# Optimization experiments

Hardware: AMD Instinct MI355X
Metric: run time of the kernel (lower is better)

Reference implementation:

```python
import jax, jax.numpy as jnp
import numpy as np

N_ATOMS = 20
N_IN, N_EMB_N, N_EMB_E, N_H_N, N_H_E = 4, 128, 128, 256, 256


def lstm_seq(x, Wi, bi, Wh, bh):
    """x: [B, M, T, D] -> h sequence [B, M, T, H]. Gates stacked as (i,f,g,o).
    Equivalent to the per-gate nn.Linear pairs: bi/bh are the two bias vectors."""
    B, M, T, D = x.shape
    H = Wh.shape[0]
    # precompute all input-to-hidden projections in one big GEMM: [T,B,M,4H]
    xg = jnp.einsum('bmtd,dg->tbmg', x, Wi) + bi

    def step(carry, xg_t):
        c, h = carry
        g = xg_t + h @ Wh + bh  # [B,M,4H]
        i, f, gg, o = jnp.split(g, 4, axis=-1)
        i = jax.nn.sigmoid(i)
        f = jax.nn.sigmoid(f)
        gg = jnp.tanh(gg)
        o = jax.nn.sigmoid(o)
        c = f * c + i * gg
        h = o * jnp.tanh(c)
        return (c, h), h

    z = jnp.zeros((B, M, H), x.dtype)
    _, hs = jax.lax.scan(step, (z, z), xg)  # hs: [T,B,M,H]
    return jnp.transpose(hs, (1, 2, 0, 3))


def setup_inputs() -> dict:
    key = jax.random.key(0)
    ks = jax.random.split(key, 16)
    s = 0.05
    # fully-connected directed edges without self loops -> one-hot incidence
    send, rec = np.where(~np.eye(N_ATOMS, dtype=bool))
    eye = np.eye(N_ATOMS, dtype=np.float32)
    inp = {
        'X': jax.random.normal(ks[0], (16, N_ATOMS, 64, N_IN), jnp.float32),
        'rel_rec': jnp.asarray(eye[rec]),
        'rel_send': jnp.asarray(eye[send]),
        # motion embedding fc
        'Wm': jax.random.normal(ks[1], (N_IN, N_EMB_N), jnp.float32) * s,
        'bm': jnp.zeros((N_EMB_N,), jnp.float32),
        # motion LSTM (gates i,f,g,o stacked)
        'Wmi': jax.random.normal(ks[2], (N_EMB_N, 4 * N_H_N), jnp.float32) * s,
        'bmi': jnp.zeros((4 * N_H_N,), jnp.float32),
        'Wmh': jax.random.normal(ks[3], (N_H_N, 4 * N_H_N), jnp.float32) * s,
        'bmh': jnp.zeros((4 * N_H_N,), jnp.float32),
        # interaction embedding fc (in = 2*n_h_node)
        'We': jax.random.normal(ks[4], (2 * N_H_N, N_EMB_E), jnp.float32) * s,
        'be': jnp.zeros((N_EMB_E,), jnp.float32),
        # edge LSTM
        'Wei': jax.random.normal(ks[5], (N_EMB_E, 4 * N_H_E), jnp.float32) * s,
        'bei': jnp.zeros((4 * N_H_E,), jnp.float32),
        'Weh': jax.random.normal(ks[6], (N_H_E, 4 * N_H_E), jnp.float32) * s,
        'beh': jnp.zeros((4 * N_H_E,), jnp.float32),
        # output fc
        'Wf': jax.random.normal(ks[7], (N_H_E, 1), jnp.float32) * s,
        'bf': jnp.zeros((1,), jnp.float32),
    }
    return inp


def reference(X, rel_rec, rel_send, Wm, bm, Wmi, bmi, Wmh, bmh,
              We, be, Wei, bei, Weh, beh, Wf, bf):
    # Motion embedding on temporal deltas: [B,N,T-1,n_emb_node]
    dX = X[:, :, 1:, :] - X[:, :, :-1, :]
    em = dX @ Wm + bm
    # Motion LSTM, full sequence: [B,N,T-1,Hn]
    hm = lstm_seq(em, Wmi, bmi, Wmh, bmh)
    # Interaction embedding: gather per-edge sender/receiver node states
    senders = jnp.einsum('en,bnth->beth', rel_send, hm)
    receivers = jnp.einsum('en,bnth->beth', rel_rec, hm)
    edges = jnp.concatenate([senders, receivers], axis=-1)  # [B,E,T-1,2Hn]
    ea = edges @ We + be  # [B,E,T-1,n_emb_edge]
    # Edge LSTM, last hidden state: [B,E,He]
    he = lstm_seq(ea, Wei, bei, Weh, beh)[:, :, -1, :]
    # Edge scores -> dense adjacency via incidence matrices
    A = jax.nn.sigmoid(he @ Wf + bf)[..., 0]  # [B,E]
    Ad = jnp.einsum('en,be,em->bnm', rel_send, A, rel_rec)  # send^T diag(A) rec
    return 0.5 * (Ad + jnp.transpose(Ad, (0, 2, 1)))  # symmetrize
```

## Files before the change

### kernel.cpp

```cpp
#include <hip/hip_runtime.h>
#include <stdint.h>

#define NBATCH 16
#define NNODE  20
#define TSTEPS 63
#define NEDGE  380
#define HID    256
#define G4     1024
#define RS     280

typedef __bf16 bf16x8 __attribute__((ext_vector_type(8)));
typedef float  f32x4  __attribute__((ext_vector_type(4)));

__device__ __forceinline__ float bf2f(unsigned short u){
  union { unsigned int i; float f; } v; v.i = ((unsigned int)u) << 16; return v.f;
}
__device__ __forceinline__ unsigned short f2bf(float f){
  union { float f; unsigned int i; } v; v.f = f;
  return (unsigned short)((v.i + 0x7FFFu + ((v.i >> 16) & 1u)) >> 16);
}
__device__ __forceinline__ bf16x8 as_frag(uint4 v){
  union { uint4 u; bf16x8 b; } c; c.u = v; return c.b;
}
__device__ __forceinline__ float sigmf(float x){ return 1.0f/(1.0f+__expf(-x)); }
__device__ __forceinline__ float tanh_f(float x){ float e=__expf(2.0f*x); return (e-1.0f)/(e+1.0f); }

__device__ __forceinline__ unsigned long long load_ax(const unsigned long long* p){
  return __hip_atomic_load(p, __ATOMIC_RELAXED, __HIP_MEMORY_SCOPE_AGENT);
}
__device__ __forceinline__ void store_ax(unsigned long long* p, unsigned long long v){
  __hip_atomic_store(p, v, __ATOMIC_RELAXED, __HIP_MEMORY_SCOPE_AGENT);
}
__device__ __forceinline__ void wait_vm0(){ asm volatile("s_waitcnt vmcnt(0)" ::: "memory"); }

__global__ __launch_bounds__(256) void prep_a(
    const float* __restrict__ We, const float* __restrict__ Wei,
    const float* __restrict__ Wm, const float* __restrict__ Wmi,
    const float* __restrict__ bm, const float* __restrict__ bmi, const float* __restrict__ bmh,
    const float* __restrict__ be, const float* __restrict__ bei, const float* __restrict__ beh,
    float* __restrict__ Wse, float* __restrict__ Wre, float* __restrict__ WcmGI,
    float* __restrict__ bcmGI, float* __restrict__ bceGI,
    float* __restrict__ Afin, unsigned int* __restrict__ ectr, unsigned int* __restrict__ mctr){
  int bid = blockIdx.x, tid = threadIdx.x;
  if (bid < 2048){
    int idx = bid*256 + tid;
    int half = idx >> 18;
    int j = idx & 262143;
    int k = j >> 10, nn = j & 1023;
    const float* Wrow = We + (half*256 + k)*128;
    float s = 0.f;
    for (int d = 0; d < 128; ++d) s += Wrow[d] * Wei[d*1024 + nn];
    (half ? Wre : Wse)[k*1024 + nn] = s;
  } else if (bid < 2064){
    int idx = (bid-2048)*256 + tid;
    int d = idx >> 10, ci = idx & 1023;
    int col = (ci & 3)*256 + (ci >> 2);
    float s = 0.f;
    for (int j = 0; j < 128; ++j) s += Wm[d*128 + j] * Wmi[j*1024 + col];
    WcmGI[idx] = s;
  } else if (bid < 2068){
    int ci = (bid-2064)*256 + tid;
    int col = (ci & 3)*256 + (ci >> 2);
    float s = bmi[col] + bmh[col];
    for (int j = 0; j < 128; ++j) s += bm[j] * Wmi[j*1024 + col];
    bcmGI[ci] = s;
  } else if (bid < 2072){
    int ci = (bid-2068)*256 + tid;
    int col = (ci & 3)*256 + (ci >> 2);
    float s = bei[col] + beh[col];
    for (int j = 0; j < 128; ++j) s += be[j] * Wei[j*1024 + col];
    bceGI[ci] = s;
  } else if (bid == 2072){
    if (tid < 64) ectr[tid] = 0u;
    else if (tid < 96) mctr[tid-64] = 0u;
  } else {
    int idx = (bid-2073)*256 + tid;
    if (idx < NBATCH*NEDGE) Afin[idx] = 0.f;
  }
}

__device__ __forceinline__ void pack_gi(const float* __restrict__ W,
                                        unsigned short* __restrict__ dst, int id){
  int lane = id & 63, kt = (id >> 6) & 7, tt = (id >> 9) & 1, w = (id >> 10) & 7, nb = id >> 13;
  int cl = lane & 15, q = lane >> 4;
  int gcol = (cl & 3)*256 + nb*64 + (w*2 + tt)*4 + (cl >> 2);
  int k0 = kt*32 + q*8;
  unsigned int wb[4];
  #pragma unroll
  for (int p = 0; p < 4; ++p){
    unsigned short a = f2bf(W[(k0+2*p  )*1024 + gcol]);
    unsigned short b = f2bf(W[(k0+2*p+1)*1024 + gcol]);
    wb[p] = (unsigned int)a | ((unsigned int)b << 16);
  }
  ((uint4*)dst)[id] = make_uint4(wb[0], wb[1], wb[2], wb[3]);
}

__device__ __forceinline__ void pack_one(const float* __restrict__ S,
                                         unsigned short* __restrict__ dst, int id, int n){
  int lane = id & 63, kt = (id >> 6) & 7;
  int k0 = kt*32 + ((lane >> 4) << 3);
  unsigned int wb[4];
  #pragma unroll
  for (int p = 0; p < 4; ++p){
    unsigned short a = f2bf(S[(k0+2*p  )*1024 + n]);
    unsigned short b = f2bf(S[(k0+2*p+1)*1024 + n]);
    wb[p] = (unsigned int)a | ((unsigned int)b << 16);
  }
  ((uint4*)dst)[id] = make_uint4(wb[0], wb[1], wb[2], wb[3]);
}

__global__ __launch_bounds__(256) void prep_b(
    const float* __restrict__ Wmh, const float* __restrict__ Weh,
    const float* __restrict__ Wse, const float* __restrict__ Wre,
    unsigned short* __restrict__ pWmh, unsigned short* __restrict__ pWeh,
    unsigned short* __restrict__ pWsr){
  int gid = blockIdx.x*256 + threadIdx.x;
  if (gid < 32768){
    pack_gi(Wmh, pWmh, gid);
  } else if (gid < 65536){
    pack_gi(Weh, pWeh, gid - 32768);
  } else {
    int id = gid - 65536;
    int ng = (id >> 9)*16 + (id & 15);
    const float* S = (ng < 1024) ? Wse : Wre;
    pack_one(S, pWsr, id, ng & 1023);
  }
}

__global__ __launch_bounds__(512, 2) void motion_lstm(
    const float* __restrict__ X, const float* __restrict__ WcmGI,
    const float* __restrict__ bcmGI, const unsigned short* __restrict__ pWmh,
    unsigned short* __restrict__ hm, unsigned short* __restrict__ mb,
    unsigned int* __restrict__ mctr){
  __shared__ __align__(16) unsigned short hst[16*RS];
  __shared__ float dxs[10*252];
  __shared__ __align__(16) float sWc[4*256];
  __shared__ __align__(16) float sbc[256];
  __shared__ __align__(16) float scr[8*2*320];
  int tid = threadIdx.x, lane = tid & 63, w = tid >> 6;
  int l15 = lane & 15, quad = lane >> 4;
  int row16 = lane >> 2, h4 = lane & 3;
  int m = blockIdx.x & 31, n = blockIdx.x >> 5;
  int s0 = m*10;
  unsigned int* ctr = mctr + m;

  uint4 wreg[2][8];
  #pragma unroll
  for (int tt = 0; tt < 2; ++tt)
    #pragma unroll
    for (int kt = 0; kt < 8; ++kt)
      wreg[tt][kt] = ((const uint4*)pWmh)[(((n*8 + w)*2 + tt)*8 + kt)*64 + lane];

  uint4 z4 = make_uint4(0,0,0,0);
  for (int i = tid; i < 560; i += 512) ((uint4*)hst)[i] = z4;
  for (int i = tid; i < 1024; i += 512) sWc[i] = WcmGI[(i >> 8)*1024 + n*256 + (i & 255)];
  if (tid < 256) sbc[tid] = bcmGI[n*256 + tid];
  for (int i = tid; i < 2520; i += 512){
    int sl = i / 252; int r = i % 252; int t = r >> 2; int d = r & 3;
    const float* Xp = X + (((size_t)(s0 + sl)*64 + t)*4 + d);
    dxs[i] = Xp[4] - Xp[0];
  }
  __syncthreads();

  float ce[2] = {0.f, 0.f};
  int sl = row16 < 10 ? row16 : 9;

  for (int t = 0; t < TSTEPS; ++t){
    if (t > 0){
      if (tid == 0){
        unsigned int tgt = 4u*(unsigned)t;
        while (__hip_atomic_load(ctr, __ATOMIC_RELAXED, __HIP_MEMORY_SCOPE_AGENT) < tgt)
          __builtin_amdgcn_s_sleep(1);
      }
      __syncthreads();
      const unsigned long long* mbp = (const unsigned long long*)
          (mb + ((size_t)((t-1)&1)*32 + m)*16*256);
      unsigned long long pv[2]; int po[2] = {-1,-1};
      #pragma unroll
      for (int j = 0; j < 2; ++j){
        int i = tid + j*512;
        if (i < 768){
          int which = i >> 8, jj = i & 255;
          int r = jj >> 4, c = jj & 15;
          int np = which + (which >= n ? 1 : 0);
          pv[j] = load_ax(&mbp[(size_t)r*64 + np*16 + c]);
          po[j] = r*RS + np*64 + c*4;
        }
      }
      #pragma unroll
      for (int j = 0; j < 2; ++j)
        if (po[j] >= 0) *(unsigned long long*)&hst[po[j]] = pv[j];
    }
    __syncthreads();

    f32x4 acc0 = {0.f,0.f,0.f,0.f}, acc1 = {0.f,0.f,0.f,0.f};
    #pragma unroll
    for (int kt = 0; kt < 8; ++kt){
      bf16x8 a = as_frag(*(const uint4*)&hst[l15*RS + kt*32 + quad*8]);
      acc0 = __builtin_amdgcn_mfma_f32_16x16x32_bf16(a, as_frag(wreg[0][kt]), acc0, 0, 0, 0);
      acc1 = __builtin_amdgcn_mfma_f32_16x16x32_bf16(a, as_frag(wreg[1][kt]), acc1, 0, 0, 0);
    }
    __syncthreads();

    int wb = w*640;
    #pragma unroll
    for (int r = 0; r < 4; ++r){
      scr[wb +       (quad*4 + r)*20 + l15] = acc0[r];
      scr[wb + 320 + (quad*4 + r)*20 + l15] = acc1[r];
    }
    #pragma unroll
    for (int tt = 0; tt < 2; ++tt){
      int tile = w*2 + tt;
      f32x4 v = *(const f32x4*)&scr[wb + tt*320 + row16*20 + h4*4];
      f32x4 bias = *(const f32x4*)&sbc[tile*16 + h4*4];
      float g0 = v[0] + bias[0], g1 = v[1] + bias[1], g2 = v[2] + bias[2], g3 = v[3] + bias[3];
      #pragma unroll
      for (int d = 0; d < 4; ++d){
        float dx = dxs[sl*252 + t*4 + d];
        f32x4 wv = *(const f32x4*)&sWc[d*256 + tile*16 + h4*4];
        g0 += dx*wv[0]; g1 += dx*wv[1]; g2 += dx*wv[2]; g3 += dx*wv[3];
      }
      float iv = sigmf(g0), fv = sigmf(g1), gv = tanh_f(g2), ov = sigmf(g3);
      float cc = fv*ce[tt] + iv*gv; ce[tt] = cc;
      hst[row16*RS + n*64 + tile*4 + h4] = f2bf(ov*tanh_f(cc));
    }
    __syncthreads();

    unsigned long long* mbc = (unsigned long long*)
        (mb + ((size_t)(t&1)*32 + m)*16*256);
    if (tid < 256){
      int r = tid >> 4, c = tid & 15;
      unsigned long long v = *(const unsigned long long*)&hst[r*RS + n*64 + c*4];
      if (t < 62) store_ax(&mbc[(size_t)r*64 + n*16 + c], v);
      if (r < 10)
        *(unsigned long long*)&hm[(((size_t)(s0 + r)*63) + t)*256 + n*64 + c*4] = v;
    }
    wait_vm0();
    __syncthreads();
    if (t < 62 && tid == 0)
      __hip_atomic_fetch_add(ctr, 1u, __ATOMIC_RELAXED, __HIP_MEMORY_SCOPE_AGENT);
  }
}

__global__ __launch_bounds__(256) void gsr_gemm(
    const unsigned short* __restrict__ hm, const unsigned short* __restrict__ pWsr,
    unsigned short* __restrict__ gsr){
  int tid = threadIdx.x, lane = tid & 63, wid = tid >> 6;
  int l15 = lane & 15, quad = lane >> 4;
  int bm = blockIdx.x % 315, bn = blockIdx.x / 315;
  int rowbase = bm*64 + (wid >> 1)*32;
  int ntbase  = bn*8  + (wid & 1)*4;
  f32x4 acc[2][4] = {};
  #pragma unroll
  for (int kt = 0; kt < 8; ++kt){
    bf16x8 af[2];
    #pragma unroll
    for (int mt = 0; mt < 2; ++mt){
      int row = rowbase + mt*16 + l15;
      af[mt] = as_frag(*(const uint4*)&hm[(size_t)row*256 + kt*32 + quad*8]);
    }
    #pragma unroll
    for (int nt = 0; nt < 4; ++nt){
      bf16x8 bfr = as_frag(*(const uint4*)&pWsr[(((size_t)(ntbase+nt)*8 + kt)*64 + lane)*8]);
      #pragma unroll
      for (int mt = 0; mt < 2; ++mt)
        acc[mt][nt] = __builtin_amdgcn_mfma_f32_16x16x32_bf16(af[mt], bfr, acc[mt][nt], 0, 0, 0);
    }
  }
  #pragma unroll
  for (int mt = 0; mt < 2; ++mt)
    #pragma unroll
    for (int nt = 0; nt < 4; ++nt){
      int col = (ntbase+nt)*16 + l15;
      int half = col >> 10, ch = col & 1023;
      int colp = (half << 10) | ((ch & 255)*4 + (ch >> 8));
      #pragma unroll
      for (int r = 0; r < 4; ++r){
        int row = rowbase + mt*16 + quad*4 + r;
        gsr[(size_t)row*2048 + colp] = f2bf(acc[mt][nt][r]);
      }
    }
}

__global__ __launch_bounds__(512, 2) void edge_lstm(
    const unsigned short* __restrict__ gsr, const float* __restrict__ bceGI,
    const unsigned short* __restrict__ pWeh, const float* __restrict__ Wf,
    unsigned short* __restrict__ hb, float* __restrict__ Afin,
    unsigned int* __restrict__ ectr){
  __shared__ __align__(16) unsigned short hst[96*RS];
  __shared__ __align__(16) unsigned short gbuf[2*25*264];
  __shared__ __align__(16) float scr[8*2*320];
  __shared__ __align__(16) float sbce[256];
  __shared__ __align__(16) float sWf[64];
  int tid = threadIdx.x, lane = tid & 63, w = tid >> 6;
  int l15 = lane & 15, quad = lane >> 4;
  int row16 = lane >> 2, h4 = lane & 3;
  int bid = blockIdx.x;
  int n = bid >> 6, G = bid & 63, b = G >> 2, m = G & 3;
  int e0 = m*95;
  unsigned int* ctr = ectr + G;

  uint4 wreg[2][8];
  #pragma unroll
  for (int tt = 0; tt < 2; ++tt)
    #pragma unroll
    for (int kt = 0; kt < 8; ++kt)
      wreg[tt][kt] = ((const uint4*)pWeh)[(((n*8 + w)*2 + tt)*8 + kt)*64 + lane];

  if (tid < 256) sbce[tid] = bceGI[n*256 + tid];
  if (tid < 64)  sWf[tid]  = Wf[n*64 + tid];
  uint4 z4 = make_uint4(0,0,0,0);
  for (int i = tid; i < 3360; i += 512) ((uint4*)hst)[i] = z4;

  int srel[6], rrec[6];
  #pragma unroll
  for (int mt = 0; mt < 6; ++mt){
    int row = mt*16 + row16;
    int e = e0 + (row < 95 ? row : 94);
    int s = e / 19; int rr = e - s*19;
    srel[mt] = s - m*5;
    rrec[mt] = rr + (rr >= s ? 1 : 0);
  }

  #pragma unroll
  for (int j = 0; j < 2; ++j){
    int i = tid + j*512;
    if (i < 800){
      int r = i >> 5, c = i & 31;
      int node = r < 5 ? m*5 + r : r - 5;
      int half = r < 5 ? 0 : 1024;
      uint4 v = *(const uint4*)&gsr[((size_t)(b*20 + node)*63)*2048 + half + n*256 + c*8];
      *(uint4*)&gbuf[r*264 + c*8] = v;
    }
  }
  __syncthreads();

  float ce[2][6]; float epi[6];
  #pragma unroll
  for (int mt = 0; mt < 6; ++mt){ ce[0][mt] = 0.f; ce[1][mt] = 0.f; epi[mt] = 0.f; }

  for (int t = 0; t < TSTEPS; ++t){
    if (t > 0){
      if (tid == 0){
        unsigned int tgt = 4u*(unsigned)t;
        while (__hip_atomic_load(ctr, __ATOMIC_RELAXED, __HIP_MEMORY_SCOPE_AGENT) < tgt)
          __builtin_amdgcn_s_sleep(1);
      }
      __syncthreads();
      const unsigned long long* hbp = (const unsigned long long*)
          (hb + (((size_t)((t-1)&1)*16 + b)*4 + m)*96*256);
      unsigned long long pv[9]; int po[9];
      #pragma unroll
      for (int j = 0; j < 9; ++j){
        int i = tid + j*512;
        int which = i / 1536, jj = i - which*1536;
        int r = jj >> 4, c = jj & 15;
        int np = which + (which >= n ? 1 : 0);
        pv[j] = load_ax(&hbp[(size_t)r*64 + np*16 + c]);
        po[j] = r*RS + np*64 + c*4;
      }
      #pragma unroll
      for (int j = 0; j < 9; ++j)
        *(unsigned long long*)&hst[po[j]] = pv[j];
    }
    if (t+1 < TSTEPS){
      #pragma unroll
      for (int j = 0; j < 2; ++j){
        int i = tid + j*512;
        if (i < 800){
          int r = i >> 5, c = i & 31;
          int node = r < 5 ? m*5 + r : r - 5;
          int half = r < 5 ? 0 : 1024;
          uint4 v = *(const uint4*)&gsr[(((size_t)(b*20 + node)*63) + (t+1))*2048 + half + n*256 + c*8];
          *(uint4*)&gbuf[((t+1)&1)*6600 + r*264 + c*8] = v;
        }
      }
    }
    __syncthreads();

    f32x4 acc[2][6];
    #pragma unroll
    for (int mt = 0; mt < 6; ++mt){ acc[0][mt] = (f32x4){0,0,0,0}; acc[1][mt] = (f32x4){0,0,0,0}; }
    #pragma unroll
    for (int kt = 0; kt < 8; ++kt){
      bf16x8 a[6];
      #pragma unroll
      for (int mt = 0; mt < 6; ++mt)
        a[mt] = as_frag(*(const uint4*)&hst[(mt*16 + l15)*RS + kt*32 + quad*8]);
      #pragma unroll
      for (int mt = 0; mt < 6; ++mt){
        acc[0][mt] = __builtin_amdgcn_mfma_f32_16x16x32_bf16(a[mt], as_frag(wreg[0][kt]), acc[0][mt], 0, 0, 0);
        acc[1][mt] = __builtin_amdgcn_mfma_f32_16x16x32_bf16(a[mt], as_frag(wreg[1][kt]), acc[1][mt], 0, 0, 0);
      }
    }
    __syncthreads();

    int bufo = (t & 1)*6600;
    int wb = w*640;
    #pragma unroll
    for (int mt = 0; mt < 6; ++mt){
      #pragma unroll
      for (int r = 0; r < 4; ++r){
        scr[wb +       (quad*4 + r)*20 + l15] = acc[0][mt][r];
        scr[wb + 320 + (quad*4 + r)*20 + l15] = acc[1][mt][r];
      }
      #pragma unroll
      for (int tt = 0; tt < 2; ++tt){
        int tile = w*2 + tt;
        int tb = tile*16 + h4*4;
        f32x4 v = *(const f32x4*)&scr[wb + tt*320 + row16*20 + h4*4];
        uint2 gs = *(const uint2*)&gbuf[bufo + srel[mt]*264 + tb];
        uint2 gr = *(const uint2*)&gbuf[bufo + (5 + rrec[mt])*264 + tb];
        f32x4 bias = *(const f32x4*)&sbce[tb];
        float g0 = v[0] + bias[0] + bf2f((unsigned short)(gs.x & 0xffff)) + bf2f((unsigned short)(gr.x & 0xffff));
        float g1 = v[1] + bias[1] + bf2f((unsigned short)(gs.x >> 16))    + bf2f((unsigned short)(gr.x >> 16));
        float g2 = v[2] + bias[2] + bf2f((unsigned short)(gs.y & 0xffff)) + bf2f((unsigned short)(gr.y & 0xffff));
        float g3 = v[3] + bias[3] + bf2f((unsigned short)(gs.y >> 16))    + bf2f((unsigned short)(gr.y >> 16));
        float iv = sigmf(g0), fv = sigmf(g1), gv = tanh_f(g2), ov = sigmf(g3);
        float cc = fv*ce[tt][mt] + iv*gv; ce[tt][mt] = cc;
        float h = ov*tanh_f(cc);
        int row = mt*16 + row16;
        if (t < 62){
          hst[row*RS + n*64 + tile*4 + h4] = f2bf(h);
        } else {
          epi[mt] += h * sWf[tile*4 + h4];
        }
      }
    }
    if (t < 62){
      __syncthreads();
      unsigned long long* hbc = (unsigned long long*)
          (hb + (((size_t)(t&1)*16 + b)*4 + m)*96*256);
      #pragma unroll
      for (int j = 0; j < 3; ++j){
        int i = tid + j*512;
        int r = i >> 4, c = i & 15;
        unsigned long long v = *(const unsigned long long*)&hst[r*RS + n*64 + c*4];
        store_ax(&hbc[(size_t)r*64 + n*16 + c], v);
      }
      wait_vm0();
      __syncthreads();
      if (tid == 0)
        __hip_atomic_fetch_add(ctr, 1u, __ATOMIC_RELAXED, __HIP_MEMORY_SCOPE_AGENT);
    }
  }
  #pragma unroll
  for (int mt = 0; mt < 6; ++mt){
    float v = epi[mt];
    v += __shfl_xor(v, 1);
    v += __shfl_xor(v, 2);
    int row = mt*16 + row16;
    if (h4 == 0 && row < 95)
      atomicAdd(&Afin[b*380 + e0 + row], v);
  }
}

__global__ __launch_bounds__(256) void finalize(const float* __restrict__ Afin,
                                                const float* __restrict__ bfp,
                                                float* __restrict__ out){
  int idx = blockIdx.x*256 + threadIdx.x;
  if (idx >= 16*400) return;
  int b = idx / 400; int ij = idx % 400; int i = ij / 20; int j = ij % 20;
  float v = 0.f;
  if (i != j){
    int e1 = i*19 + j - (j > i ? 1 : 0);
    int e2 = j*19 + i - (i > j ? 1 : 0);
    float bf = bfp[0];
    v = 0.5f*(sigmf(Afin[b*380 + e1] + bf) + sigmf(Afin[b*380 + e2] + bf));
  }
  out[idx] = v;
}

extern "C" void kernel_launch(void* const* d_in, const int* in_sizes, int n_in,
                              void* d_out, int out_size, void* d_ws, size_t ws_size,
                              hipStream_t stream){
  (void)in_sizes; (void)n_in; (void)out_size; (void)ws_size;
  const float* X   = (const float*)d_in[0];
  const float* Wm  = (const float*)d_in[3];
  const float* bm  = (const float*)d_in[4];
  const float* Wmi = (const float*)d_in[5];
  const float* bmi = (const float*)d_in[6];
  const float* Wmh = (const float*)d_in[7];
  const float* bmh = (const float*)d_in[8];
  const float* We  = (const float*)d_in[9];
  const float* be  = (const float*)d_in[10];
  const float* Wei = (const float*)d_in[11];
  const float* bei = (const float*)d_in[12];
  const float* Weh = (const float*)d_in[13];
  const float* beh = (const float*)d_in[14];
  const float* Wf  = (const float*)d_in[15];
  const float* bfp = (const float*)d_in[16];

  char* ws = (char*)d_ws;
  float* Wse   = (float*)(ws + 0);
  float* Wre   = (float*)(ws + 1048576);
  float* WcmGI = (float*)(ws + 2097152);
  float* bcmGI = (float*)(ws + 2113536);
  float* bceGI = (float*)(ws + 2117632);
  unsigned short* pWmh = (unsigned short*)(ws + 2121728);
  unsigned short* pWeh = (unsigned short*)(ws + 2646016);
  unsigned short* pWsr = (unsigned short*)(ws + 3170304);
  unsigned short* hm   = (unsigned short*)(ws + 4218880);
  unsigned short* gsr  = (unsigned short*)(ws + 14540800);
  unsigned short* hb   = (unsigned short*)(ws + 97116160);
  unsigned short* mb   = hb;
  float* Afin          = (float*)(ws + 103407616);
  unsigned int* ectr   = (unsigned int*)(ws + 103432192);
  unsigned int* mctr   = (unsigned int*)(ws + 103432448);
  float* out = (float*)d_out;

  hipLaunchKernelGGL(prep_a, dim3(2097), dim3(256), 0, stream,
                     We, Wei, Wm, Wmi, bm, bmi, bmh, be, bei, beh,
                     Wse, Wre, WcmGI, bcmGI, bceGI, Afin, ectr, mctr);
  hipLaunchKernelGGL(prep_b, dim3(512), dim3(256), 0, stream,
                     Wmh, Weh, Wse, Wre, pWmh, pWeh, pWsr);
  {
    void* margs[] = {(void*)&X, (void*)&WcmGI, (void*)&bcmGI, (void*)&pWmh,
                     (void*)&hm, (void*)&mb, (void*)&mctr};
    hipLaunchCooperativeKernel(reinterpret_cast<void*>(motion_lstm),
                               dim3(128), dim3(512), margs, 0, stream);
  }
  hipLaunchKernelGGL(gsr_gemm, dim3(315*16), dim3(256), 0, stream,
                     hm, pWsr, gsr);
  {
    void* eargs[] = {(void*)&gsr, (void*)&bceGI, (void*)&pWeh, (void*)&Wf,
                     (void*)&hb, (void*)&Afin, (void*)&ectr};
    hipLaunchCooperativeKernel(reinterpret_cast<void*>(edge_lstm),
                               dim3(256), dim3(512), eargs, 0, stream);
  }
  hipLaunchKernelGGL(finalize, dim3(25), dim3(256), 0, stream,
                     Afin, bfp, out);
}
```

Before: 1.158 ms.

## Restructure LSTM step sync: per-wave counters, double-buffered state, in-register gate transpose

Both recurrent LSTM kernels now double-buffer the hidden-state tile in LDS, so most per-step __syncthreads can go. Each wave publishes its own slice and bumps a per-(group,block) counter, and every thread polls the four counters instead of one thread spinning. Gate values are rearranged in registers with a shuffle-based 4x4 transpose instead of a shared-memory scratch round trip, and the bias is preloaded into the accumulators. In the edge kernel, the sender/receiver input-gate gather becomes an extra MFMA against a one-hot A fragment. The cost is more LDS, more global polling traffic, and subtle ordering risks in the per-wave publishing.

After: 2.175 ms. 87.9% more time.

```diff
diff --git a/kernel.cpp b/kernel.cpp
--- a/kernel.cpp
+++ b/kernel.cpp
@@ -6,7 +6,6 @@
 #define TSTEPS 63
 #define NEDGE  380
 #define HID    256
-#define G4     1024
 #define RS     280
 
 typedef __bf16 bf16x8 __attribute__((ext_vector_type(8)));
@@ -31,7 +30,23 @@
 __device__ __forceinline__ void store_ax(unsigned long long* p, unsigned long long v){
   __hip_atomic_store(p, v, __ATOMIC_RELAXED, __HIP_MEMORY_SCOPE_AGENT);
 }
+__device__ __forceinline__ unsigned int load_ax32(const unsigned int* p){
+  return __hip_atomic_load(p, __ATOMIC_RELAXED, __HIP_MEMORY_SCOPE_AGENT);
+}
 __device__ __forceinline__ void wait_vm0(){ asm volatile("s_waitcnt vmcnt(0)" ::: "memory"); }
+
+__device__ __forceinline__ void xpose4(f32x4& v, int cl){
+  float s0 = __shfl_xor((float)v[1], 1), s1 = __shfl_xor((float)v[0], 1);
+  float s2 = __shfl_xor((float)v[3], 1), s3 = __shfl_xor((float)v[2], 1);
+  bool b0 = (cl & 1);
+  float a0 = b0 ? s0 : v[0], a1 = b0 ? v[1] : s1;
+  float a2 = b0 ? s2 : v[2], a3 = b0 ? v[3] : s3;
+  float t0 = __shfl_xor(a2, 2), t1 = __shfl_xor(a3, 2);
+  float t2 = __shfl_xor(a0, 2), t3 = __shfl_xor(a1, 2);
+  bool b1 = (cl & 2);
+  v[0] = b1 ? t0 : a0; v[1] = b1 ? t1 : a1;
+  v[2] = b1 ? a2 : t2; v[3] = b1 ? a3 : t3;
+}
 
 __global__ __launch_bounds__(256) void prep_a(
     const float* __restrict__ We, const float* __restrict__ Wei,
@@ -71,8 +86,8 @@
     for (int j = 0; j < 128; ++j) s += be[j] * Wei[j*1024 + col];
     bceGI[ci] = s;
   } else if (bid == 2072){
-    if (tid < 64) ectr[tid] = 0u;
-    else if (tid < 96) mctr[tid-64] = 0u;
+    ectr[tid] = 0u;
+    if (tid < 128) mctr[tid] = 0u;
   } else {
     int idx = (bid-2073)*256 + tid;
     if (idx < NBATCH*NEDGE) Afin[idx] = 0.f;
@@ -132,17 +147,15 @@
     const float* __restrict__ bcmGI, const unsigned short* __restrict__ pWmh,
     unsigned short* __restrict__ hm, unsigned short* __restrict__ mb,
     unsigned int* __restrict__ mctr){
-  __shared__ __align__(16) unsigned short hst[16*RS];
+  __shared__ __align__(16) unsigned short hst[2][16*RS];
   __shared__ float dxs[10*252];
   __shared__ __align__(16) float sWc[4*256];
   __shared__ __align__(16) float sbc[256];
-  __shared__ __align__(16) float scr[8*2*320];
   int tid = threadIdx.x, lane = tid & 63, w = tid >> 6;
   int l15 = lane & 15, quad = lane >> 4;
-  int row16 = lane >> 2, h4 = lane & 3;
   int m = blockIdx.x & 31, n = blockIdx.x >> 5;
   int s0 = m*10;
-  unsigned int* ctr = mctr + m;
+  unsigned int* ctrs = mctr + m*4;
 
   uint4 wreg[2][8];
   #pragma unroll
@@ -152,7 +165,7 @@
       wreg[tt][kt] = ((const uint4*)pWmh)[(((n*8 + w)*2 + tt)*8 + kt)*64 + lane];
 
   uint4 z4 = make_uint4(0,0,0,0);
-  for (int i = tid; i < 560; i += 512) ((uint4*)hst)[i] = z4;
+  for (int i = tid; i < 1120; i += 512) ((uint4*)hst)[i] = z4;
   for (int i = tid; i < 1024; i += 512) sWc[i] = WcmGI[(i >> 8)*1024 + n*256 + (i & 255)];
   if (tid < 256) sbc[tid] = bcmGI[n*256 + tid];
   for (int i = tid; i < 2520; i += 512){
@@ -162,19 +175,24 @@
   }
   __syncthreads();
 
+  float bb[2] = { sbc[(w*2+0)*16 + l15], sbc[(w*2+1)*16 + l15] };
+  int row = quad*4 + (l15 & 3);
+  int hsub = l15 >> 2;
+  int slr = row < 10 ? row : 9;
   float ce[2] = {0.f, 0.f};
-  int sl = row16 < 10 ? row16 : 9;
 
   for (int t = 0; t < TSTEPS; ++t){
+    int par = t & 1, nxt = par ^ 1;
     if (t > 0){
-      if (tid == 0){
-        unsigned int tgt = 4u*(unsigned)t;
-        while (__hip_atomic_load(ctr, __ATOMIC_RELAXED, __HIP_MEMORY_SCOPE_AGENT) < tgt)
-          __builtin_amdgcn_s_sleep(1);
-      }
-      __syncthreads();
-      const unsigned long long* mbp = (const unsigned long long*)
-          (mb + ((size_t)((t-1)&1)*32 + m)*16*256);
+      unsigned int tgt = 8u*(unsigned)t;
+      while (1){
+        unsigned int c0 = load_ax32(ctrs+0), c1 = load_ax32(ctrs+1);
+        unsigned int c2 = load_ax32(ctrs+2), c3 = load_ax32(ctrs+3);
+        if (c0 >= tgt && c1 >= tgt && c2 >= tgt && c3 >= tgt) break;
+        __builtin_amdgcn_s_sleep(1);
+      }
+      const unsigned long long* mbp = (const unsigned long long*)mb
+          + ((size_t)((t-1)&1)*32 + m)*16*64;
       unsigned long long pv[2]; int po[2] = {-1,-1};
       #pragma unroll
       for (int j = 0; j < 2; ++j){
@@ -189,56 +207,51 @@
       }
       #pragma unroll
       for (int j = 0; j < 2; ++j)
-        if (po[j] >= 0) *(unsigned long long*)&hst[po[j]] = pv[j];
+        if (po[j] >= 0) *(unsigned long long*)&hst[par][po[j]] = pv[j];
     }
     __syncthreads();
 
-    f32x4 acc0 = {0.f,0.f,0.f,0.f}, acc1 = {0.f,0.f,0.f,0.f};
+    f32x4 acc[2];
+    acc[0] = (f32x4){bb[0],bb[0],bb[0],bb[0]};
+    acc[1] = (f32x4){bb[1],bb[1],bb[1],bb[1]};
     #pragma unroll
     for (int kt = 0; kt < 8; ++kt){
-      bf16x8 a = as_frag(*(const uint4*)&hst[l15*RS + kt*32 + quad*8]);
-      acc0 = __builtin_amdgcn_mfma_f32_16x16x32_bf16(a, as_frag(wreg[0][kt]), acc0, 0, 0, 0);
-      acc1 = __builtin_amdgcn_mfma_f32_16x16x32_bf16(a, as_frag(wreg[1][kt]), acc1, 0, 0, 0);
-    }
-    __syncthreads();
-
-    int wb = w*640;
-    #pragma unroll
-    for (int r = 0; r < 4; ++r){
-      scr[wb +       (quad*4 + r)*20 + l15] = acc0[r];
-      scr[wb + 320 + (quad*4 + r)*20 + l15] = acc1[r];
-    }
+      bf16x8 a = as_frag(*(const uint4*)&hst[par][l15*RS + kt*32 + quad*8]);
+      acc[0] = __builtin_amdgcn_mfma_f32_16x16x32_bf16(a, as_frag(wreg[0][kt]), acc[0], 0, 0, 0);
+      acc[1] = __builtin_amdgcn_mfma_f32_16x16x32_bf16(a, as_frag(wreg[1][kt]), acc[1], 0, 0, 0);
+    }
+
+    f32x4 dxv = *(const f32x4*)&dxs[slr*252 + t*4];
     #pragma unroll
     for (int tt = 0; tt < 2; ++tt){
-      int tile = w*2 + tt;
-      f32x4 v = *(const f32x4*)&scr[wb + tt*320 + row16*20 + h4*4];
-      f32x4 bias = *(const f32x4*)&sbc[tile*16 + h4*4];
-      float g0 = v[0] + bias[0], g1 = v[1] + bias[1], g2 = v[2] + bias[2], g3 = v[3] + bias[3];
+      int tl = w*2 + tt;
+      f32x4 v = acc[tt];
+      xpose4(v, l15);
       #pragma unroll
       for (int d = 0; d < 4; ++d){
-        float dx = dxs[sl*252 + t*4 + d];
-        f32x4 wv = *(const f32x4*)&sWc[d*256 + tile*16 + h4*4];
-        g0 += dx*wv[0]; g1 += dx*wv[1]; g2 += dx*wv[2]; g3 += dx*wv[3];
-      }
-      float iv = sigmf(g0), fv = sigmf(g1), gv = tanh_f(g2), ov = sigmf(g3);
-      float cc = fv*ce[tt] + iv*gv; ce[tt] = cc;
-      hst[row16*RS + n*64 + tile*4 + h4] = f2bf(ov*tanh_f(cc));
-    }
-    __syncthreads();
-
-    unsigned long long* mbc = (unsigned long long*)
-        (mb + ((size_t)(t&1)*32 + m)*16*256);
-    if (tid < 256){
-      int r = tid >> 4, c = tid & 15;
-      unsigned long long v = *(const unsigned long long*)&hst[r*RS + n*64 + c*4];
-      if (t < 62) store_ax(&mbc[(size_t)r*64 + n*16 + c], v);
-      if (r < 10)
-        *(unsigned long long*)&hm[(((size_t)(s0 + r)*63) + t)*256 + n*64 + c*4] = v;
-    }
-    wait_vm0();
-    __syncthreads();
-    if (t < 62 && tid == 0)
-      __hip_atomic_fetch_add(ctr, 1u, __ATOMIC_RELAXED, __HIP_MEMORY_SCOPE_AGENT);
+        f32x4 wv = *(const f32x4*)&sWc[d*256 + tl*16 + hsub*4];
+        v[0] += dxv[d]*wv[0]; v[1] += dxv[d]*wv[1];
+        v[2] += dxv[d]*wv[2]; v[3] += dxv[d]*wv[3];
+      }
+      float iv = sigmf(v[0]), fv = sigmf(v[1]), gg = tanh_f(v[2]), ov = sigmf(v[3]);
+      float cc = fv*ce[tt] + iv*gg; ce[tt] = cc;
+      unsigned short hb16 = f2bf(ov*tanh_f(cc));
+      if (t < 62) hst[nxt][row*RS + n*64 + tl*4 + hsub] = hb16;
+      if (row < 10)
+        hm[(((size_t)(s0 + row)*63) + t)*256 + n*64 + tl*4 + hsub] = hb16;
+    }
+    if (t < 62){
+      unsigned long long* mbc = (unsigned long long*)mb
+          + ((size_t)(t&1)*32 + m)*16*64;
+      if (lane < 32){
+        int tlg = lane >> 4, r = lane & 15;
+        unsigned long long v = *(const unsigned long long*)&hst[nxt][r*RS + n*64 + (w*2+tlg)*4];
+        store_ax(&mbc[(size_t)r*64 + n*16 + w*2 + tlg], v);
+      }
+      wait_vm0();
+      if ((tid & 63) == 0)
+        __hip_atomic_fetch_add(&ctrs[n], 1u, __ATOMIC_RELAXED, __HIP_MEMORY_SCOPE_AGENT);
+    }
   }
 }
 
@@ -256,8 +269,8 @@
     bf16x8 af[2];
     #pragma unroll
     for (int mt = 0; mt < 2; ++mt){
-      int row = rowbase + mt*16 + l15;
-      af[mt] = as_frag(*(const uint4*)&hm[(size_t)row*256 + kt*32 + quad*8]);
+      int r = rowbase + mt*16 + l15;
+      af[mt] = as_frag(*(const uint4*)&hm[(size_t)r*256 + kt*32 + quad*8]);
     }
     #pragma unroll
     for (int nt = 0; nt < 4; ++nt){
@@ -280,6 +293,26 @@
         gsr[(size_t)row*2048 + colp] = f2bf(acc[mt][nt][r]);
       }
     }
+}
+
+__device__ __forceinline__ void stage_gxb(const unsigned short* __restrict__ gsr,
+                                          unsigned short* __restrict__ gxbuf,
+                                          int tid, int b, int m, int n, int tq){
+  for (int i = tid; i < 400; i += 512){
+    int kk = i >> 4, c8 = i & 15;
+    int node = kk < 5 ? m*5 + kk : kk - 5;
+    int off  = kk < 5 ? 0 : 1024;
+    uint4 v = *(const uint4*)&gsr[((size_t)(b*20 + node)*63 + tq)*2048 + off + n*256 + c8*8];
+    unsigned short* bp = &gxbuf[(c8>>1)*512 + (c8&1)*256 + kk];
+    bp[0]   = (unsigned short)(v.x);
+    bp[32]  = (unsigned short)(v.x >> 16);
+    bp[64]  = (unsigned short)(v.y);
+    bp[96]  = (unsigned short)(v.y >> 16);
+    bp[128] = (unsigned short)(v.z);
+    bp[160] = (unsigned short)(v.z >> 16);
+    bp[192] = (unsigned short)(v.w);
+    bp[224] = (unsigned short)(v.w >> 16);
+  }
 }
 
 __global__ __launch_bounds__(512, 2) void edge_lstm(
@@ -287,18 +320,16 @@
     const unsigned short* __restrict__ pWeh, const float* __restrict__ Wf,
     unsigned short* __restrict__ hb, float* __restrict__ Afin,
     unsigned int* __restrict__ ectr){
-  __shared__ __align__(16) unsigned short hst[96*RS];
-  __shared__ __align__(16) unsigned short gbuf[2*25*264];
-  __shared__ __align__(16) float scr[8*2*320];
+  __shared__ __align__(16) unsigned short hst[2][96*RS];
+  __shared__ __align__(16) unsigned short gxb[2][8192];
   __shared__ __align__(16) float sbce[256];
   __shared__ __align__(16) float sWf[64];
   int tid = threadIdx.x, lane = tid & 63, w = tid >> 6;
   int l15 = lane & 15, quad = lane >> 4;
-  int row16 = lane >> 2, h4 = lane & 3;
   int bid = blockIdx.x;
   int n = bid >> 6, G = bid & 63, b = G >> 2, m = G & 3;
   int e0 = m*95;
-  unsigned int* ctr = ectr + G;
+  unsigned int* ctrs = ectr + G*4;
 
   uint4 wreg[2][8];
   #pragma unroll
@@ -306,49 +337,54 @@
     #pragma unroll
     for (int kt = 0; kt < 8; ++kt)
       wreg[tt][kt] = ((const uint4*)pWeh)[(((n*8 + w)*2 + tt)*8 + kt)*64 + lane];
+
+  uint4 aoh[6];
+  #pragma unroll
+  for (int mt = 0; mt < 6; ++mt){
+    int row = mt*16 + l15;
+    int e = e0 + (row < 95 ? row : 94);
+    int s = e / 19; int rr = e - s*19;
+    int sr = s - m*5;
+    int rc = rr + (rr >= s ? 1 : 0);
+    unsigned int wd[4];
+    #pragma unroll
+    for (int p = 0; p < 4; ++p){
+      int k0 = quad*8 + 2*p, k1 = k0 + 1;
+      unsigned short a0 = ((k0 < 5) ? (sr == k0) : (k0 < 25 && rc == k0-5)) ? 0x3F80 : 0;
+      unsigned short a1 = ((k1 < 5) ? (sr == k1) : (k1 < 25 && rc == k1-5)) ? 0x3F80 : 0;
+      wd[p] = (unsigned int)a0 | ((unsigned int)a1 << 16);
+    }
+    aoh[mt] = make_uint4(wd[0], wd[1], wd[2], wd[3]);
+  }
 
   if (tid < 256) sbce[tid] = bceGI[n*256 + tid];
   if (tid < 64)  sWf[tid]  = Wf[n*64 + tid];
   uint4 z4 = make_uint4(0,0,0,0);
-  for (int i = tid; i < 3360; i += 512) ((uint4*)hst)[i] = z4;
-
-  int srel[6], rrec[6];
-  #pragma unroll
-  for (int mt = 0; mt < 6; ++mt){
-    int row = mt*16 + row16;
-    int e = e0 + (row < 95 ? row : 94);
-    int s = e / 19; int rr = e - s*19;
-    srel[mt] = s - m*5;
-    rrec[mt] = rr + (rr >= s ? 1 : 0);
-  }
-
-  #pragma unroll
-  for (int j = 0; j < 2; ++j){
-    int i = tid + j*512;
-    if (i < 800){
-      int r = i >> 5, c = i & 31;
-      int node = r < 5 ? m*5 + r : r - 5;
-      int half = r < 5 ? 0 : 1024;
-      uint4 v = *(const uint4*)&gsr[((size_t)(b*20 + node)*63)*2048 + half + n*256 + c*8];
-      *(uint4*)&gbuf[r*264 + c*8] = v;
-    }
-  }
+  for (int i = tid; i < 13440; i += 512) ((uint4*)hst)[i] = z4;
+  for (int i = tid; i < 2048; i += 512) ((uint4*)gxb)[i] = z4;
   __syncthreads();
 
+  float bb[2]  = { sbce[(w*2+0)*16 + l15], sbce[(w*2+1)*16 + l15] };
+  float wfr[2] = { sWf[(w*2+0)*4 + (l15>>2)], sWf[(w*2+1)*4 + (l15>>2)] };
+
+  stage_gxb(gsr, &gxb[0][0], tid, b, m, n, 0);
+
   float ce[2][6]; float epi[6];
   #pragma unroll
   for (int mt = 0; mt < 6; ++mt){ ce[0][mt] = 0.f; ce[1][mt] = 0.f; epi[mt] = 0.f; }
 
   for (int t = 0; t < TSTEPS; ++t){
+    int par = t & 1, nxt = par ^ 1;
     if (t > 0){
-      if (tid == 0){
-        unsigned int tgt = 4u*(unsigned)t;
-        while (__hip_atomic_load(ctr, __ATOMIC_RELAXED, __HIP_MEMORY_SCOPE_AGENT) < tgt)
-          __builtin_amdgcn_s_sleep(1);
-      }
-      __syncthreads();
-      const unsigned long long* hbp = (const unsigned long long*)
-          (hb + (((size_t)((t-1)&1)*16 + b)*4 + m)*96*256);
+      unsigned int tgt = 8u*(unsigned)t;
+      while (1){
+        unsigned int c0 = load_ax32(ctrs+0), c1 = load_ax32(ctrs+1);
+        unsigned int c2 = load_ax32(ctrs+2), c3 = load_ax32(ctrs+3);
+        if (c0 >= tgt && c1 >= tgt && c2 >= tgt && c3 >= tgt) break;
+        __builtin_amdgcn_s_sleep(1);
+      }
+      const unsigned long long* hbp = (const unsigned long long*)hb
+          + (((size_t)((t-1)&1)*16 + b)*4 + m)*96*64;
       unsigned long long pv[9]; int po[9];
       #pragma unroll
       for (int j = 0; j < 9; ++j){
@@ -361,97 +397,83 @@
       }
       #pragma unroll
       for (int j = 0; j < 9; ++j)
-        *(unsigned long long*)&hst[po[j]] = pv[j];
-    }
-    if (t+1 < TSTEPS){
-      #pragma unroll
-      for (int j = 0; j < 2; ++j){
-        int i = tid + j*512;
-        if (i < 800){
-          int r = i >> 5, c = i & 31;
-          int node = r < 5 ? m*5 + r : r - 5;
-          int half = r < 5 ? 0 : 1024;
-          uint4 v = *(const uint4*)&gsr[(((size_t)(b*20 + node)*63) + (t+1))*2048 + half + n*256 + c*8];
-          *(uint4*)&gbuf[((t+1)&1)*6600 + r*264 + c*8] = v;
-        }
-      }
-    }
+        *(unsigned long long*)&hst[par][po[j]] = pv[j];
+    }
+    if (t + 1 < TSTEPS)
+      stage_gxb(gsr, &gxb[nxt][0], tid, b, m, n, t+1);
     __syncthreads();
 
     f32x4 acc[2][6];
     #pragma unroll
-    for (int mt = 0; mt < 6; ++mt){ acc[0][mt] = (f32x4){0,0,0,0}; acc[1][mt] = (f32x4){0,0,0,0}; }
+    for (int mt = 0; mt < 6; ++mt){
+      acc[0][mt] = (f32x4){bb[0],bb[0],bb[0],bb[0]};
+      acc[1][mt] = (f32x4){bb[1],bb[1],bb[1],bb[1]};
+    }
     #pragma unroll
     for (int kt = 0; kt < 8; ++kt){
       bf16x8 a[6];
       #pragma unroll
       for (int mt = 0; mt < 6; ++mt)
-        a[mt] = as_frag(*(const uint4*)&hst[(mt*16 + l15)*RS + kt*32 + quad*8]);
+        a[mt] = as_frag(*(const uint4*)&hst[par][(mt*16 + l15)*RS + kt*32 + quad*8]);
       #pragma unroll
       for (int mt = 0; mt < 6; ++mt){
         acc[0][mt] = __builtin_amdgcn_mfma_f32_16x16x32_bf16(a[mt], as_frag(wreg[0][kt]), acc[0][mt], 0, 0, 0);
         acc[1][mt] = __builtin_amdgcn_mfma_f32_16x16x32_bf16(a[mt], as_frag(wreg[1][kt]), acc[1][mt], 0, 0, 0);
       }
     }
-    __syncthreads();
-
-    int bufo = (t & 1)*6600;
-    int wb = w*640;
-    #pragma unroll
-    for (int mt = 0; mt < 6; ++mt){
-      #pragma unroll
-      for (int r = 0; r < 4; ++r){
-        scr[wb +       (quad*4 + r)*20 + l15] = acc[0][mt][r];
-        scr[wb + 320 + (quad*4 + r)*20 + l15] = acc[1][mt][r];
-      }
-      #pragma unroll
-      for (int tt = 0; tt < 2; ++tt){
-        int tile = w*2 + tt;
-        int tb = tile*16 + h4*4;
-        f32x4 v = *(const f32x4*)&scr[wb + tt*320 + row16*20 + h4*4];
-        uint2 gs = *(const uint2*)&gbuf[bufo + srel[mt]*264 + tb];
-        uint2 gr = *(const uint2*)&gbuf[bufo + (5 + rrec[mt])*264 + tb];
-        f32x4 bias = *(const f32x4*)&sbce[tb];
-        float g0 = v[0] + bias[0] + bf2f((unsigned short)(gs.x & 0xffff)) + bf2f((unsigned short)(gr.x & 0xffff));
-        float g1 = v[1] + bias[1] + bf2f((unsigned short)(gs.x >> 16))    + bf2f((unsigned short)(gr.x >> 16));
-        float g2 = v[2] + bias[2] + bf2f((unsigned short)(gs.y & 0xffff)) + bf2f((unsigned short)(gr.y & 0xffff));
-        float g3 = v[3] + bias[3] + bf2f((unsigned short)(gs.y >> 16))    + bf2f((unsigned short)(gr.y >> 16));
-        float iv = sigmf(g0), fv = sigmf(g1), gv = tanh_f(g2), ov = sigmf(g3);
-        float cc = fv*ce[tt][mt] + iv*gv; ce[tt][mt] = cc;
+    {
+      bf16x8 bx0 = as_frag(*(const uint4*)&gxb[par][(w*2+0)*512 + l15*32 + quad*8]);
+      bf16x8 bx1 = as_frag(*(const uint4*)&gxb[par][(w*2+1)*512 + l15*32 + quad*8]);
+      #pragma unroll
+      for (int mt = 0; mt < 6; ++mt){
+        acc[0][mt] = __builtin_amdgcn_mfma_f32_16x16x32_bf16(as_frag(aoh[mt]), bx0, acc[0][mt], 0, 0, 0);
+        acc[1][mt] = __builtin_amdgcn_mfma_f32_16x16x32_bf16(as_frag(aoh[mt]), bx1, acc[1][mt], 0, 0, 0);
+      }
+    }
+
+    #pragma unroll
+    for (int tt = 0; tt < 2; ++tt){
+      int tl = w*2 + tt;
+      #pragma unroll
+      for (int mt = 0; mt < 6; ++mt){
+        f32x4 v = acc[tt][mt];
+        xpose4(v, l15);
+        float iv = sigmf(v[0]), fv = sigmf(v[1]), gg = tanh_f(v[2]), ov = sigmf(v[3]);
+        float cc = fv*ce[tt][mt] + iv*gg; ce[tt][mt] = cc;
         float h = ov*tanh_f(cc);
-        int row = mt*16 + row16;
         if (t < 62){
-          hst[row*RS + n*64 + tile*4 + h4] = f2bf(h);
+          int row = mt*16 + quad*4 + (l15 & 3);
+          hst[nxt][row*RS + n*64 + tl*4 + (l15>>2)] = f2bf(h);
         } else {
-          epi[mt] += h * sWf[tile*4 + h4];
+          epi[mt] += h * wfr[tt];
         }
       }
     }
     if (t < 62){
-      __syncthreads();
-      unsigned long long* hbc = (unsigned long long*)
-          (hb + (((size_t)(t&1)*16 + b)*4 + m)*96*256);
-      #pragma unroll
-      for (int j = 0; j < 3; ++j){
-        int i = tid + j*512;
-        int r = i >> 4, c = i & 15;
-        unsigned long long v = *(const unsigned long long*)&hst[r*RS + n*64 + c*4];
-        store_ax(&hbc[(size_t)r*64 + n*16 + c], v);
+      unsigned long long* hbc = (unsigned long long*)hb
+          + (((size_t)(t&1)*16 + b)*4 + m)*96*64;
+      #pragma unroll
+      for (int k = 0; k < 3; ++k){
+        int idx = lane + k*64;
+        int tlg = idx / 96, r = idx - tlg*96;
+        unsigned long long v = *(const unsigned long long*)&hst[nxt][r*RS + n*64 + (w*2+tlg)*4];
+        store_ax(&hbc[(size_t)r*64 + n*16 + w*2 + tlg], v);
       }
       wait_vm0();
-      __syncthreads();
-      if (tid == 0)
-        __hip_atomic_fetch_add(ctr, 1u, __ATOMIC_RELAXED, __HIP_MEMORY_SCOPE_AGENT);
+      if ((tid & 63) == 0)
+        __hip_atomic_fetch_add(&ctrs[n], 1u, __ATOMIC_RELAXED, __HIP_MEMORY_SCOPE_AGENT);
     }
   }
   #pragma unroll
   for (int mt = 0; mt < 6; ++mt){
     float v = epi[mt];
-    v += __shfl_xor(v, 1);
-    v += __shfl_xor(v, 2);
-    int row = mt*16 + row16;
-    if (h4 == 0 && row < 95)
-      atomicAdd(&Afin[b*380 + e0 + row], v);
+    v += __shfl_xor(v, 4);
+    v += __shfl_xor(v, 8);
+    if (l15 < 4){
+      int row = mt*16 + quad*4 + l15;
+      if (row < 95)
+        atomicAdd(&Afin[b*380 + e0 + row], v);
+    }
   }
 }
 
@@ -506,7 +528,7 @@
   unsigned short* mb   = hb;
   float* Afin          = (float*)(ws + 103407616);
   unsigned int* ectr   = (unsigned int*)(ws + 103432192);
-  unsigned int* mctr   = (unsigned int*)(ws + 103432448);
+  unsigned int* mctr   = (unsigned int*)(ws + 103433216);
   float* out = (float*)d_out;
 
   hipLaunchKernelGGL(prep_a, dim3(2097), dim3(256), 0, stream,
```
